# Optimization experiments

Hardware: AMD Instinct MI355X
Metric: run time of the kernel (lower is better)

## Reference

```python
import jax, jax.numpy as jnp
import numpy as np

EPS_NORM = 1e-5
EPS_L2 = 1e-12
SCALE_VALUE = 50.0
FROM_VALUE = 0.4
VALUE_INTERVAL = 0.5


def mvn(x):
    # mean-variance norm per (b, c) over spatial dims; torch .var() is unbiased
    mean = jnp.mean(x, axis=(2, 3), keepdims=True)
    var = jnp.var(x, axis=(2, 3), keepdims=True, ddof=1)
    return (x - mean) / jnp.sqrt(var + EPS_NORM)


def conv1x1(x, W, b):
    # x: [b,c,h,w], W: [out,in], b: [out]
    return jnp.einsum('bchw,oc->bohw', x, W) + b[None, :, None, None]


def setup_inputs() -> dict:
    key = jax.random.key(0)
    ks = jax.random.split(key, 12)
    B, C, Hs, Ws = 4, 512, 64, 64
    HW = Hs * Ws  # 4096 == spatial_dims
    HID = HW // 16
    sc = 1.0 / np.sqrt(C)
    inp = {
        'content': jax.random.normal(ks[0], (B, C, Hs, Ws), jnp.float32),
        'style': jax.random.normal(ks[1], (B, C, Hs, Ws), jnp.float32),
        'Wf': jax.random.normal(ks[2], (C, C), jnp.float32) * sc,
        'bf': jnp.zeros((C,), jnp.float32),
        'Wg': jax.random.normal(ks[3], (C, C), jnp.float32) * sc,
        'bg': jnp.zeros((C,), jnp.float32),
        'Wh': jax.random.normal(ks[4], (C, C), jnp.float32) * sc,
        'bh': jnp.zeros((C,), jnp.float32),
        'Wout': jax.random.normal(ks[5], (C, C), jnp.float32) * sc,
        'bout': jnp.zeros((C,), jnp.float32),
        'W1': jax.random.normal(ks[6], (HID, HW), jnp.float32) * (1.0 / np.sqrt(HW)),
        'b1': jnp.zeros((HID,), jnp.float32),
        'W2': jax.random.normal(ks[7], (1, HID), jnp.float32) * (1.0 / np.sqrt(HID)),
        'b2': jnp.zeros((1,), jnp.float32),
    }
    return inp


def reference(content, style, Wf, bf, Wg, bg, Wh, bh, Wout, bout, W1, b1, W2, b2):
    B, C, H, W = content.shape
    HW = H * W

    Fq = conv1x1(mvn(content), Wf, bf).reshape(B, C, HW)   # query feats
    Gk = conv1x1(mvn(style), Wg, bg).reshape(B, C, HW)      # key feats
    Hv = conv1x1(style, Wh, bh).reshape(B, C, HW)           # value feats

    # affinity matrix: channel-L2-normalized cosine similarity [B, HW_c, HW_s]
    cf = content.reshape(B, C, HW)
    sf = style.reshape(B, C, HW)
    cf = cf / jnp.maximum(jnp.linalg.norm(cf, axis=1, keepdims=True), EPS_L2)
    sf = sf / jnp.maximum(jnp.linalg.norm(sf, axis=1, keepdims=True), EPS_L2)
    A = jnp.einsum('bck,bcl->bkl', cf, sf)

    # attention scores + softmax over style positions
    S = jax.nn.softmax(jnp.einsum('bck,bcl->bkl', Fq, Gk), axis=-1)

    # AEAModule: per-content-pixel adaptive clamp from affinity rows
    hmid = jnp.einsum('bkl,ol->bko', A, W1) + b1            # [B, HW, HID]
    hmid = jax.nn.leaky_relu(hmid, 0.2)
    psi = jax.nn.sigmoid(jnp.einsum('bko,po->bkp', hmid, W2) + b2)  # [B, HW, 1]
    clamp_value = psi * VALUE_INTERVAL + FROM_VALUE
    Sg = jax.nn.sigmoid(SCALE_VALUE * (S - clamp_value))    # gated attention

    # O = H @ Sg^T : [B, C, HW_c]
    O = jnp.einsum('bcl,bkl->bck', Hv, Sg).reshape(B, C, H, W)
    O = conv1x1(O, Wout, bout) + content
    return O
```

## Files before the change

### kernel.cpp

```cpp
#include <hip/hip_runtime.h>

typedef unsigned short u16;
typedef __attribute__((ext_vector_type(8))) short short8;
typedef __attribute__((ext_vector_type(4))) float f32x4;

static constexpr int Bn  = 4;
static constexpr int C   = 512;
static constexpr int HW  = 4096;
static constexpr int HID = 256;

__device__ __forceinline__ float bf2f(u16 u){
  union { unsigned int i; float f; } x; x.i = ((unsigned int)u) << 16; return x.f;
}
__device__ __forceinline__ u16 f2bf(float f){
  union { float f; unsigned int i; } x; x.f = f;
  return (u16)((x.i + 0x7fffu + ((x.i >> 16) & 1u)) >> 16);
}
__device__ __forceinline__ void gld16(const u16* g, u16* l){
  __builtin_amdgcn_global_load_lds((const __attribute__((address_space(1))) void*)g,
                                   (__attribute__((address_space(3))) void*)l, 16, 0, 0);
}

template<bool SPLIT>
__device__ __forceinline__ void mfma_core(const u16* __restrict__ Ah, const u16* __restrict__ Al, int pA,
                                          const u16* __restrict__ Bh, const u16* __restrict__ Bl, int pB,
                                          int K, u16* lds, f32x4 (&acc)[4][4]){
  const int tid  = threadIdx.x;
  const int lane = tid & 63, wave = tid >> 6;
  const int fr = lane & 15, kq = lane >> 4;
  const int kqs = (kq ^ ((fr >> 1) & 3)) * 8;
  const int wm = (wave & 1) * 64, wn = (wave >> 1) * 64;
  constexpr int HB = SPLIT ? 16384 : 8192;
  const int srow = wave*32 + (lane >> 2);
  const int sq   = (((lane & 3) ^ ((lane >> 3) & 3))) * 8;
  const size_t ga = (size_t)srow * pA + sq;
  const size_t gb = (size_t)srow * pB + sq;
  const int ldsc = wave * 1024;

  auto stage = [&](int buf, int k0){
    u16* L = lds + buf*HB;
    #pragma unroll
    for (int i = 0; i < 2; ++i){
      gld16(Ah + ga + (size_t)i*16*pA + k0, L + ldsc + i*512);
      gld16(Bh + gb + (size_t)i*16*pB + k0, L + 4096 + ldsc + i*512);
      if constexpr (SPLIT){
        gld16(Al + ga + (size_t)i*16*pA + k0, L + 8192  + ldsc + i*512);
        gld16(Bl + gb + (size_t)i*16*pB + k0, L + 12288 + ldsc + i*512);
      }
    }
  };
  auto compute = [&](int buf){
    u16* L = lds + buf*HB;
    short8 a[4], b[4];
    #pragma unroll
    for (int i = 0; i < 4; ++i){
      a[i] = *(const short8*)&L[(wm + i*16 + fr)*32 + kqs];
      b[i] = *(const short8*)&L[4096 + (wn + i*16 + fr)*32 + kqs];
    }
    #pragma unroll
    for (int i = 0; i < 4; ++i)
      #pragma unroll
      for (int j = 0; j < 4; ++j)
        acc[i][j] = __builtin_amdgcn_mfma_f32_16x16x32_bf16(a[i], b[j], acc[i][j], 0, 0, 0);
    if constexpr (SPLIT){
      short8 a2[4], b2[4];
      #pragma unroll
      for (int i = 0; i < 4; ++i){
        a2[i] = *(const short8*)&L[8192  + (wm + i*16 + fr)*32 + kqs];
        b2[i] = *(const short8*)&L[12288 + (wn + i*16 + fr)*32 + kqs];
      }
      #pragma unroll
      for (int i = 0; i < 4; ++i)
        #pragma unroll
        for (int j = 0; j < 4; ++j){
          acc[i][j] = __builtin_amdgcn_mfma_f32_16x16x32_bf16(a[i],  b2[j], acc[i][j], 0, 0, 0);
          acc[i][j] = __builtin_amdgcn_mfma_f32_16x16x32_bf16(a2[i], b[j],  acc[i][j], 0, 0, 0);
        }
    }
  };

  stage(0, 0);
  int cur = 0;
  for (int k0 = 32; k0 < K; k0 += 32){
    stage(cur ^ 1, k0);
    if constexpr (SPLIT) asm volatile("s_waitcnt vmcnt(8)" ::: "memory");
    else                 asm volatile("s_waitcnt vmcnt(4)" ::: "memory");
    __builtin_amdgcn_s_barrier();
    compute(cur);
    __builtin_amdgcn_s_barrier();
    cur ^= 1;
  }
  asm volatile("s_waitcnt vmcnt(0)" ::: "memory");
  __builtin_amdgcn_s_barrier();
  compute(cur);
}

struct TileCtx { int wm, wn, cn, rq; };
__device__ __forceinline__ TileCtx tctx(){
  TileCtx t;
  const int wave = threadIdx.x >> 6, lane = threadIdx.x & 63;
  t.wm = blockIdx.y * 128 + (wave & 1) * 64;
  t.wn = blockIdx.x * 128 + (wave >> 1) * 64;
  t.cn = lane & 15; t.rq = (lane >> 4) * 4;
  return t;
}
#define ACC_ZERO(acc) { _Pragma("unroll") for (int i=0;i<4;++i) _Pragma("unroll") for (int j=0;j<4;++j) _Pragma("unroll") for (int r=0;r<4;++r) acc[i][j][r]=0.f; }

__global__ __launch_bounds__(256) void g_conv_split2(const u16* __restrict__ A0h, const u16* __restrict__ A0l,
                                                     const u16* __restrict__ A1h, const u16* __restrict__ A1l,
                                                     const u16* __restrict__ B0h, const u16* __restrict__ B0l,
                                                     const u16* __restrict__ B1h, const u16* __restrict__ B1l,
                                                     const float* __restrict__ bias0, const float* __restrict__ bias1,
                                                     u16* __restrict__ O0h, u16* __restrict__ O0l,
                                                     u16* __restrict__ O1h, u16* __restrict__ O1l,
                                                     size_t bsA, size_t bsO){
  __shared__ u16 lds[32768];
  const int zb = blockIdx.z, b = zb >> 1, z = zb & 1;
  const u16* Ah = (z ? A1h : A0h) + (size_t)b*bsA;  const u16* Al = (z ? A1l : A0l) + (size_t)b*bsA;
  const u16* Bh = z ? B1h : B0h;  const u16* Bl = z ? B1l : B0l;
  const float* bias = z ? bias1 : bias0;
  u16* Ohi = (z ? O1h : O0h) + (size_t)b*bsO;  u16* Olo = (z ? O1l : O0l) + (size_t)b*bsO;
  TileCtx t = tctx();
  f32x4 acc[4][4]; ACC_ZERO(acc);
  mfma_core<true>(Ah + (size_t)blockIdx.y*128*C, Al + (size_t)blockIdx.y*128*C, C,
                  Bh + (size_t)blockIdx.x*128*C, Bl + (size_t)blockIdx.x*128*C, C, C, lds, acc);
  #pragma unroll
  for (int fm = 0; fm < 4; ++fm)
    #pragma unroll
    for (int fn = 0; fn < 4; ++fn)
      #pragma unroll
      for (int r = 0; r < 4; ++r){
        int gm = t.wm + fm*16 + t.rq + r;
        int gn = t.wn + fn*16 + t.cn;
        float v = acc[fm][fn][r] + bias[gn];
        u16 h = f2bf(v);
        Ohi[(size_t)gm*C + gn] = h;
        Olo[(size_t)gm*C + gn] = f2bf(v - bf2f(h));
      }
}

__global__ __launch_bounds__(256) void g_gemm_split_f32(const u16* __restrict__ Ah, const u16* __restrict__ Al, int pA,
                                                        const u16* __restrict__ Bh, const u16* __restrict__ Bl, int pB,
                                                        int K, float* __restrict__ O, int pO,
                                                        size_t bsA, size_t bsB, size_t bsO){
  __shared__ u16 lds[32768];
  const int b = blockIdx.z;
  TileCtx t = tctx();
  f32x4 acc[4][4]; ACC_ZERO(acc);
  mfma_core<true>(Ah + (size_t)b*bsA + (size_t)blockIdx.y*128*pA,
                  Al + (size_t)b*bsA + (size_t)blockIdx.y*128*pA, pA,
                  Bh + (size_t)b*bsB + (size_t)blockIdx.x*128*pB,
                  Bl + (size_t)b*bsB + (size_t)blockIdx.x*128*pB, pB, K, lds, acc);
  float* Ob = O + (size_t)b*bsO;
  #pragma unroll
  for (int fm = 0; fm < 4; ++fm)
    #pragma unroll
    for (int fn = 0; fn < 4; ++fn)
      #pragma unroll
      for (int r = 0; r < 4; ++r)
        Ob[(size_t)(t.wm + fm*16 + t.rq + r)*pO + t.wn + fn*16 + t.cn] = acc[fm][fn][r];
}

__global__ __launch_bounds__(256) void g_gemm_biasm_bf16(const u16* __restrict__ A, int pA,
                                                         const u16* __restrict__ B, int pB,
                                                         int K, const float* __restrict__ bias,
                                                         u16* __restrict__ O, int pO,
                                                         size_t bsB, size_t bsO){
  __shared__ u16 lds[16384];
  const int b = blockIdx.z;
  TileCtx t = tctx();
  f32x4 acc[4][4]; ACC_ZERO(acc);
  mfma_core<false>(A + (size_t)blockIdx.y*128*pA, nullptr, pA,
                   B + (size_t)b*bsB + (size_t)blockIdx.x*128*pB, nullptr, pB, K, lds, acc);
  u16* Ob = O + (size_t)b*bsO;
  #pragma unroll
  for (int fm = 0; fm < 4; ++fm)
    #pragma unroll
    for (int fn = 0; fn < 4; ++fn)
      #pragma unroll
      for (int r = 0; r < 4; ++r){
        int gm = t.wm + fm*16 + t.rq + r;
        Ob[(size_t)gm*pO + t.wn + fn*16 + t.cn] = f2bf(acc[fm][fn][r] + bias[gm]);
      }
}

__global__ __launch_bounds__(256) void g_gemm_plain_bf16(const u16* __restrict__ A, int pA,
                                                         const u16* __restrict__ B, int pB,
                                                         int K, u16* __restrict__ O, int pO,
                                                         size_t bsA, size_t bsB, size_t bsO){
  __shared__ u16 lds[16384];
  const int b = blockIdx.z;
  TileCtx t = tctx();
  f32x4 acc[4][4]; ACC_ZERO(acc);
  mfma_core<false>(A + (size_t)b*bsA + (size_t)blockIdx.y*128*pA, nullptr, pA,
                   B + (size_t)b*bsB + (size_t)blockIdx.x*128*pB, nullptr, pB, K, lds, acc);
  u16* Ob = O + (size_t)b*bsO;
  #pragma unroll
  for (int fm = 0; fm < 4; ++fm)
    #pragma unroll
    for (int fn = 0; fn < 4; ++fn)
      #pragma unroll
      for (int r = 0; r < 4; ++r){
        int gm = t.wm + fm*16 + t.rq + r;
        Ob[(size_t)gm*pO + t.wn + fn*16 + t.cn] = f2bf(acc[fm][fn][r]);
      }
}

__global__ __launch_bounds__(256) void g_gemm_partial(const u16* __restrict__ A, int pA,
                                                      const u16* __restrict__ B, int pB,
                                                      int Kper, float* __restrict__ O, int pO,
                                                      size_t sliceStride, int slices,
                                                      size_t bsB, size_t bsO){
  __shared__ u16 lds[16384];
  const int zz = blockIdx.z;
  const int b = zz / slices, sl = zz - b*slices;
  TileCtx t = tctx();
  const int koff = sl * Kper;
  f32x4 acc[4][4]; ACC_ZERO(acc);
  mfma_core<false>(A + (size_t)blockIdx.y*128*pA + koff, nullptr, pA,
                   B + (size_t)b*bsB + (size_t)blockIdx.x*128*pB + koff, nullptr, pB, Kper, lds, acc);
  float* Oz = O + (size_t)b*bsO + (size_t)sl * sliceStride;
  #pragma unroll
  for (int fm = 0; fm < 4; ++fm)
    #pragma unroll
    for (int fn = 0; fn < 4; ++fn)
      #pragma unroll
      for (int r = 0; r < 4; ++r)
        Oz[(size_t)(t.wm + fm*16 + t.rq + r)*pO + t.wn + fn*16 + t.cn] = acc[fm][fn][r];
}

__global__ __launch_bounds__(256) void k_reduce(const float* __restrict__ in, size_t sliceStride,
                                                int S, u16* __restrict__ out,
                                                size_t bsIn, size_t bsOut){
  const int b = blockIdx.y;
  const float* inb = in + (size_t)b*bsIn;
  u16* outb = out + (size_t)b*bsOut;
  const size_t i4 = ((size_t)blockIdx.x*256 + threadIdx.x) * 4;
  float4 s = *(const float4*)&inb[i4];
  for (int z = 1; z < S; ++z){
    float4 v = *(const float4*)&inb[(size_t)z*sliceStride + i4];
    s.x += v.x; s.y += v.y; s.z += v.z; s.w += v.w;
  }
  u16 r0 = f2bf(s.x), r1 = f2bf(s.y), r2 = f2bf(s.z), r3 = f2bf(s.w);
  uint2 uo; uo.x = (unsigned)r0 | ((unsigned)r1 << 16);
  uo.y = (unsigned)r2 | ((unsigned)r3 << 16);
  *(uint2*)&outb[i4] = uo;
}

__global__ __launch_bounds__(256) void g_gemm_outconv(const u16* __restrict__ A, int pA,
                                                      const u16* __restrict__ B, int pB,
                                                      int K, const float* __restrict__ bias,
                                                      const float* __restrict__ res,
                                                      float* __restrict__ O,
                                                      size_t bsB, size_t bsRes, size_t bsO){
  __shared__ u16 lds[16384];
  const int b = blockIdx.z;
  TileCtx t = tctx();
  f32x4 acc[4][4]; ACC_ZERO(acc);
  mfma_core<false>(A + (size_t)blockIdx.y*128*pA, nullptr, pA,
                   B + (size_t)b*bsB + (size_t)blockIdx.x*128*pB, nullptr, pB, K, lds, acc);
  const float* resb = res + (size_t)b*bsRes;
  float* Ob = O + (size_t)b*bsO;
  #pragma unroll
  for (int fm = 0; fm < 4; ++fm)
    #pragma unroll
    for (int fn = 0; fn < 4; ++fn)
      #pragma unroll
      for (int r = 0; r < 4; ++r){
        int gm = t.wm + fm*16 + t.rq + r;
        int gn = t.wn + fn*16 + t.cn;
        Ob[(size_t)gm*HW + gn] = acc[fm][fn][r] + bias[gm] + resb[(size_t)gm*HW + gn];
      }
}

__global__ __launch_bounds__(256) void g_gemm_hmid(const u16* __restrict__ A, int pA,
                                                   const u16* __restrict__ B, int pB,
                                                   int K, const float* __restrict__ inc,
                                                   const float* __restrict__ b1,
                                                   float* __restrict__ O,
                                                   size_t bsA, size_t bsP, size_t bsInc, size_t bsO){
  __shared__ u16 lds[16384];
  const int b = blockIdx.z;
  TileCtx t = tctx();
  f32x4 acc[4][4]; ACC_ZERO(acc);
  mfma_core<false>(A + (size_t)b*bsA + (size_t)blockIdx.y*128*pA, nullptr, pA,
                   B + (size_t)b*bsP + (size_t)blockIdx.x*128*pB, nullptr, pB, K, lds, acc);
  const float* incb = inc + (size_t)b*bsInc;
  float* Ob = O + (size_t)b*bsO;
  #pragma unroll
  for (int fm = 0; fm < 4; ++fm)
    #pragma unroll
    for (int fn = 0; fn < 4; ++fn)
      #pragma unroll
      for (int r = 0; r < 4; ++r){
        int gm = t.wm + fm*16 + t.rq + r;
        int gn = t.wn + fn*16 + t.cn;
        float h = acc[fm][fn][r] * incb[gm] + b1[gn];
        Ob[(size_t)gm*HID + gn] = (h > 0.f) ? h : 0.2f*h;
      }
}

__global__ __launch_bounds__(256) void k_stats(const float* __restrict__ content,
                                               const float* __restrict__ style,
                                               float2* __restrict__ statsC,
                                               float2* __restrict__ statsS){
  const int bc = blockIdx.x;
  const float* X = (blockIdx.y == 0 ? content : style) + (size_t)bc * HW;
  float s = 0.f, sq = 0.f;
  for (int i = threadIdx.x; i < HW; i += 256){ float v = X[i]; s += v; sq += v*v; }
  __shared__ float rs[256], rq[256];
  rs[threadIdx.x] = s; rq[threadIdx.x] = sq; __syncthreads();
  for (int o = 128; o > 0; o >>= 1){
    if (threadIdx.x < o){ rs[threadIdx.x] += rs[threadIdx.x+o]; rq[threadIdx.x] += rq[threadIdx.x+o]; }
    __syncthreads();
  }
  if (threadIdx.x == 0){
    float mean = rs[0] / (float)HW;
    float var  = (rq[0] - rs[0]*mean) / (float)(HW - 1);
    (blockIdx.y == 0 ? statsC : statsS)[bc] = make_float2(mean, rsqrtf(var + 1e-5f));
  }
}

__global__ __launch_bounds__(256) void k_pixnorm(const float* __restrict__ content,
                                                 const float* __restrict__ style,
                                                 float* __restrict__ inc,
                                                 float* __restrict__ ins){
  const int b = blockIdx.y;
  const int k = blockIdx.x * 256 + threadIdx.x;
  const float* X = (blockIdx.z == 0 ? content : style) + (size_t)b * C * HW + k;
  float acc = 0.f;
  for (int c = 0; c < C; ++c){ float v = X[(size_t)c * HW]; acc += v*v; }
  (blockIdx.z == 0 ? inc : ins)[b*HW + k] = 1.f / fmaxf(sqrtf(acc), 1e-12f);
}

__global__ __launch_bounds__(256) void k_prep2(const float* __restrict__ Xc,
                                               const float* __restrict__ Xs,
                                               const float2* __restrict__ stC,
                                               const float2* __restrict__ stSt,
                                               const float* __restrict__ ins,
                                               u16* __restrict__ ThiC, u16* __restrict__ TloC, u16* __restrict__ TrawC,
                                               u16* __restrict__ ThiS, u16* __restrict__ TloS, u16* __restrict__ TrawS,
                                               u16* __restrict__ stSo,
                                               size_t bsX, size_t bsT, int bsSt, size_t bsIns, size_t bsSo){
  const int zb = blockIdx.z, b = zb >> 1, z = zb & 1;
  const float* X = (z ? Xs : Xc) + (size_t)b*bsX;
  const float2* stats = (z ? stSt : stC) + (size_t)b*bsSt;
  u16* Thi = (z ? ThiS : ThiC) + (size_t)b*bsT;
  u16* Tlo = (z ? TloS : TloC) + (size_t)b*bsT;
  u16* Traw = (z ? TrawS : TrawC) + (size_t)b*bsT;
  u16* sSb = stSo + (size_t)b*bsSo;
  const float* insb = ins + (size_t)b*bsIns;
  __shared__ float tile[64][65];
  __shared__ float2 st[64];
  const int k0 = blockIdx.x*64, c0 = blockIdx.y*64;
  const int t = threadIdx.x;
  if (t < 64) st[t] = stats[c0 + t];
  const int j4 = (t & 15) * 4, i0 = t >> 4;
  float4 sv;
  if (z) sv = *(const float4*)&insb[k0 + j4];
  for (int r = 0; r < 4; ++r){
    int i = i0 + r*16;
    float4 v = *(const float4*)&X[(size_t)(c0+i)*HW + k0 + j4];
    tile[i][j4+0] = v.x; tile[i][j4+1] = v.y; tile[i][j4+2] = v.z; tile[i][j4+3] = v.w;
    if (z){
      u16 q0 = f2bf(v.x*sv.x), q1 = f2bf(v.y*sv.y), q2 = f2bf(v.z*sv.z), q3 = f2bf(v.w*sv.w);
      uint2 uo; uo.x = (unsigned)q0 | ((unsigned)q1 << 16);
      uo.y = (unsigned)q2 | ((unsigned)q3 << 16);
      *(uint2*)&sSb[(size_t)(c0+i)*HW + k0 + j4] = uo;
    }
  }
  __syncthreads();
  const int kk = t >> 2, cc = (t & 3) * 16;
  u16 h[16], l[16], rw[16];
  #pragma unroll
  for (int q = 0; q < 16; ++q){
    float x = tile[cc+q][kk];
    float2 s = st[cc+q];
    rw[q] = f2bf(x);
    float v = (x - s.x) * s.y;
    h[q] = f2bf(v);
    l[q] = f2bf(v - bf2f(h[q]));
  }
  size_t o = (size_t)(k0+kk)*C + c0 + cc;
  #pragma unroll
  for (int q = 0; q < 16; ++q){ Thi[o+q] = h[q]; Tlo[o+q] = l[q]; Traw[o+q] = rw[q]; }
}

__global__ __launch_bounds__(256) void k_wprep(const float* __restrict__ Wf, const float* __restrict__ Wg,
                                               const float* __restrict__ Wh, const float* __restrict__ Wo,
                                               const float* __restrict__ W1,
                                               u16* __restrict__ Wfh, u16* __restrict__ Wfl,
                                               u16* __restrict__ Wgh, u16* __restrict__ Wgl,
                                               u16* __restrict__ Whb, u16* __restrict__ Wob,
                                               u16* __restrict__ W1b){
  const int idx = (blockIdx.x*256 + threadIdx.x) * 4;
  const int mode = blockIdx.y;
  const int nsmall = C*C;
  if (mode == 4){
    float4 v = *(const float4*)&W1[idx];
    W1b[idx+0]=f2bf(v.x); W1b[idx+1]=f2bf(v.y); W1b[idx+2]=f2bf(v.z); W1b[idx+3]=f2bf(v.w);
    return;
  }
  if (idx >= nsmall) return;
  const float* src = (mode==0)?Wf:(mode==1)?Wg:(mode==2)?Wh:Wo;
  float4 v = *(const float4*)&src[idx];
  float vv[4] = {v.x, v.y, v.z, v.w};
  if (mode <= 1){
    u16* oh = (mode==0)?Wfh:Wgh;  u16* ol = (mode==0)?Wfl:Wgl;
    #pragma unroll
    for (int q = 0; q < 4; ++q){
      u16 hh = f2bf(vv[q]);
      oh[idx+q] = hh; ol[idx+q] = f2bf(vv[q] - bf2f(hh));
    }
  } else {
    u16* ob = (mode==2)?Whb:Wob;
    #pragma unroll
    for (int q = 0; q < 4; ++q) ob[idx+q] = f2bf(vv[q]);
  }
}

__global__ __launch_bounds__(256) void k_psi(const float* __restrict__ hmid,
                                             const float* __restrict__ W2,
                                             const float* __restrict__ b2,
                                             float* __restrict__ clampv,
                                             size_t bsH, size_t bsC){
  const int k = blockIdx.x, tid = threadIdx.x, b = blockIdx.y;
  __shared__ float red[256];
  red[tid] = hmid[(size_t)b*bsH + (size_t)k*HID + tid] * W2[tid];
  __syncthreads();
  for (int o = 128; o > 0; o >>= 1){
    if (tid < o) red[tid] += red[tid+o];
    __syncthreads();
  }
  if (tid == 0){
    float psi = 1.f/(1.f + __expf(-(red[0] + b2[0])));
    clampv[(size_t)b*bsC + k] = psi*0.5f + 0.4f;
  }
}

__global__ __launch_bounds__(256) void k_softgate(float* __restrict__ T2,
                                                  const float* __restrict__ clampv,
                                                  size_t bsT, size_t bsC){
  const int k = blockIdx.x, tid = threadIdx.x, b = blockIdx.y;
  float* row = &T2[(size_t)b*bsT + (size_t)k*HW];
  float vals[16];
  float mx = -3.4e38f;
  #pragma unroll
  for (int i = 0; i < 16; ++i){ vals[i] = row[tid + i*256]; mx = fmaxf(mx, vals[i]); }
  __shared__ float red[256];
  red[tid] = mx; __syncthreads();
  for (int o = 128; o > 0; o >>= 1){
    if (tid < o) red[tid] = fmaxf(red[tid], red[tid+o]);
    __syncthreads();
  }
  mx = red[0]; __syncthreads();
  float s = 0.f;
  #pragma unroll
  for (int i = 0; i < 16; ++i){ vals[i] = __expf(vals[i] - mx); s += vals[i]; }
  red[tid] = s; __syncthreads();
  for (int o = 128; o > 0; o >>= 1){
    if (tid < o) red[tid] += red[tid+o];
    __syncthreads();
  }
  const float inv = 1.f / red[0];
  const float cv = clampv[(size_t)b*bsC + k];
  u16* Sg = (u16*)row;
  #pragma unroll
  for (int i = 0; i < 16; ++i){
    float sg = 1.f/(1.f + __expf(-50.f*(vals[i]*inv - cv)));
    Sg[tid + i*256] = f2bf(sg);
  }
}

extern "C" void kernel_launch(void* const* d_in, const int* in_sizes, int n_in,
                              void* d_out, int out_size, void* d_ws, size_t ws_size,
                              hipStream_t stream){
  const float* content = (const float*)d_in[0];
  const float* style   = (const float*)d_in[1];
  const float* Wf   = (const float*)d_in[2];  const float* bfv  = (const float*)d_in[3];
  const float* Wg   = (const float*)d_in[4];  const float* bg   = (const float*)d_in[5];
  const float* Wh   = (const float*)d_in[6];  const float* bh   = (const float*)d_in[7];
  const float* Wo   = (const float*)d_in[8];  const float* bout = (const float*)d_in[9];
  const float* W1   = (const float*)d_in[10]; const float* b1   = (const float*)d_in[11];
  const float* W2   = (const float*)d_in[12]; const float* b2   = (const float*)d_in[13];
  float* out = (float*)d_out;
  (void)in_sizes; (void)n_in; (void)out_size;

  char* ws = (char*)d_ws;
  size_t off = 0;
  auto alloc = [&](size_t bytes)->void*{
    void* p = (void*)(ws + off);
    off += (bytes + 255) & ~(size_t)255;
    return p;
  };
  float2* statsC = (float2*)alloc((size_t)Bn*C*sizeof(float2));
  float2* statsS = (float2*)alloc((size_t)Bn*C*sizeof(float2));
  float*  inc    = (float*) alloc((size_t)Bn*HW*sizeof(float));
  float*  ins    = (float*) alloc((size_t)Bn*HW*sizeof(float));
  float*  clampv = (float*) alloc((size_t)Bn*HW*sizeof(float));
  u16* Wfh = (u16*)alloc((size_t)C*C*2), *Wfl = (u16*)alloc((size_t)C*C*2);
  u16* Wgh = (u16*)alloc((size_t)C*C*2), *Wgl = (u16*)alloc((size_t)C*C*2);
  u16* Whb = (u16*)alloc((size_t)C*C*2), *Wob = (u16*)alloc((size_t)C*C*2);
  u16* W1b = (u16*)alloc((size_t)HID*HW*2);
  const size_t commonEnd = off;

  const size_t TPB = (size_t)HW*C;
  const size_t XB  = (size_t)C*HW;
  const size_t SLB = (size_t)Bn*TPB*2;

  k_stats  <<<dim3(Bn*C, 2),       256, 0, stream>>>(content, style, statsC, statsS);
  k_pixnorm<<<dim3(HW/256, Bn, 2), 256, 0, stream>>>(content, style, inc, ins);
  k_wprep  <<<dim3(HID*HW/1024, 5),256, 0, stream>>>(Wf, Wg, Wh, Wo, W1,
                                                     Wfh, Wfl, Wgh, Wgl, Whb, Wob, W1b);

  auto runPrep = [&](char* R, u16* bFqTh, u16* bFqTl, u16* bGkTh, u16* bGkTl,
                     u16* bHvb, u16* bPT){
    u16* bXcTh = (u16*)(R + 0*SLB);
    u16* bXcTl = (u16*)(R + 1*SLB);
    u16* bXsTh = (u16*)(R + 2*SLB);
    u16* bXsTl = (u16*)(R + 3*SLB);
    u16* bCrT  = (u16*)(R + 4*SLB);
    u16* bSrT  = (u16*)(R + 5*SLB);
    u16* bstS  = (u16*)(R + 6*SLB);
    float* bPpart = (float*)(R + 0*SLB);
    float* bhmid  = (float*)(R + 1*SLB);
    k_prep2 <<<dim3(HW/64, C/64, 2*Bn), 256, 0, stream>>>(content, style, statsC, statsS, ins,
                                                          bXcTh, bXcTl, bCrT, bXsTh, bXsTl, bSrT,
                                                          bstS, XB, TPB, C, HW, TPB);
    g_conv_split2<<<dim3(C/128, HW/128, 2*Bn), 256, 0, stream>>>(
        bXcTh, bXcTl, bXsTh, bXsTl, Wfh, Wfl, Wgh, Wgl, bfv, bg,
        bFqTh, bFqTl, bGkTh, bGkTl, TPB, TPB);
    g_gemm_biasm_bf16<<<dim3(HW/128, C/128, Bn), 256, 0, stream>>>(Whb, C, bSrT, C, C, bh,
                                                                   bHvb, HW, TPB, TPB);
    g_gemm_partial<<<dim3(C/128, HID/128, Bn*8), 256, 0, stream>>>(W1b, HW, bstS, HW, HW/8,
                                                                   bPpart, C, (size_t)HID*C, 8,
                                                                   TPB, (size_t)8*HID*C);
    k_reduce<<<dim3(HID*C/1024, Bn), 256, 0, stream>>>(bPpart, (size_t)HID*C, 8, bPT,
                                                       (size_t)8*HID*C, (size_t)HID*C);
    g_gemm_hmid<<<dim3(HID/128, HW/128, Bn), 256, 0, stream>>>(bCrT, C, bPT, C, C, inc, b1, bhmid,
                                                               TPB, (size_t)HID*C, HW, (size_t)HW*HID);
    k_psi<<<dim3(HW, Bn), 256, 0, stream>>>(bhmid, W2, b2, clampv, (size_t)HW*HID, HW);
  };

  {
    size_t o = commonEnd;
    auto al = [&](size_t bytes)->void*{ void* p = (void*)(ws + o); o += (bytes + 255) & ~(size_t)255; return p; };
    u16* bFqTh = (u16*)al(SLB), *bFqTl = (u16*)al(SLB);
    u16* bGkTh = (u16*)al(SLB), *bGkTl = (u16*)al(SLB);
    u16* bHvb  = (u16*)al(SLB);
    u16* bPT   = (u16*)al((size_t)Bn*HID*C*2);
    u16* bO1T  = (u16*)al(SLB);
    char* R    = (char*)al((size_t)Bn*HW*HW*4);
    if (o <= ws_size){
      runPrep(R, bFqTh, bFqTl, bGkTh, bGkTl, bHvb, bPT);
      float* bT2 = (float*)R;
      g_gemm_split_f32<<<dim3(HW/128, HW/128, Bn), 256, 0, stream>>>(bFqTh, bFqTl, C, bGkTh, bGkTl, C,
                                                                     C, bT2, HW,
                                                                     TPB, TPB, (size_t)HW*HW);
      k_softgate<<<dim3(HW, Bn), 256, 0, stream>>>(bT2, clampv, (size_t)HW*HW, HW);
      g_gemm_plain_bf16<<<dim3(C/128, HW/128, Bn), 256, 0, stream>>>((const u16*)bT2, 2*HW, bHvb, HW,
                                                                     HW, bO1T, C,
                                                                     (size_t)HW*HW*2, TPB, TPB);
      g_gemm_outconv<<<dim3(HW/128, C/128, Bn), 256, 0, stream>>>(Wob, C, bO1T, C, C, bout, content, out,
                                                                  TPB, XB, XB);
      return;
    }
  }

  {
    size_t o = commonEnd;
    auto al = [&](size_t bytes)->void*{ void* p = (void*)(ws + o); o += (bytes + 255) & ~(size_t)255; return p; };
    u16* bFqTh = (u16*)al(SLB), *bFqTl = (u16*)al(SLB);
    u16* bGkTh = (u16*)al(SLB), *bGkTl = (u16*)al(SLB);
    u16* bHvb  = (u16*)al(SLB);
    u16* bPT   = (u16*)al((size_t)Bn*HID*C*2);
    char* R    = (char*)al((size_t)2*HW*HW*4 + (size_t)2*TPB*2 + 256);
    if (o <= ws_size){
      runPrep(R, bFqTh, bFqTl, bGkTh, bGkTl, bHvb, bPT);
      float* T2s  = (float*)R;
      u16*   O1Ts = (u16*)(R + (size_t)2*HW*HW*4);
      for (int cb = 0; cb < Bn; cb += 2){
        g_gemm_split_f32<<<dim3(HW/128, HW/128, 2), 256, 0, stream>>>(
            bFqTh + (size_t)cb*TPB, bFqTl + (size_t)cb*TPB, C,
            bGkTh + (size_t)cb*TPB, bGkTl + (size_t)cb*TPB, C, C, T2s, HW,
            TPB, TPB, (size_t)HW*HW);
        k_softgate<<<dim3(HW, 2), 256, 0, stream>>>(T2s, clampv + (size_t)cb*HW,
                                                    (size_t)HW*HW, HW);
        g_gemm_plain_bf16<<<dim3(C/128, HW/128, 2), 256, 0, stream>>>(
            (const u16*)T2s, 2*HW, bHvb + (size_t)cb*TPB, HW, HW, O1Ts, C,
            (size_t)HW*HW*2, TPB, TPB);
        g_gemm_outconv<<<dim3(HW/128, C/128, 2), 256, 0, stream>>>(
            Wob, C, O1Ts, C, C, bout, content + (size_t)cb*XB, out + (size_t)cb*XB,
            TPB, XB, XB);
      }
      return;
    }
  }

  {
    size_t o = commonEnd;
    auto al = [&](size_t bytes)->void*{ void* p = (void*)(ws + o); o += (bytes + 255) & ~(size_t)255; return p; };
    u16* bFqTh = (u16*)al(SLB), *bFqTl = (u16*)al(SLB);
    u16* bGkTh = (u16*)al(SLB), *bGkTl = (u16*)al(SLB);
    u16* bHvb  = (u16*)al(SLB);
    u16* bPT   = (u16*)al((size_t)Bn*HID*C*2);
    char* R    = (char*)al(7*SLB);
    if (o <= ws_size){
      runPrep(R, bFqTh, bFqTl, bGkTh, bGkTl, bHvb, bPT);
      float* T2s   = (float*)(R + 0*SLB);
      float* Opart = (float*)(R + 4*SLB);
      u16*   O1Ts  = (u16*)  (R + 6*SLB);
      for (int b = 0; b < Bn; ++b){
        g_gemm_split_f32<<<dim3(HW/128, HW/128), 256, 0, stream>>>(
            bFqTh + (size_t)b*TPB, bFqTl + (size_t)b*TPB, C,
            bGkTh + (size_t)b*TPB, bGkTl + (size_t)b*TPB, C, C, T2s, HW, 0, 0, 0);
        k_softgate<<<dim3(HW), 256, 0, stream>>>(T2s, clampv + (size_t)b*HW, 0, 0);
        g_gemm_partial<<<dim3(C/128, HW/128, 4), 256, 0, stream>>>(
            (const u16*)T2s, 2*HW, bHvb + (size_t)b*TPB, HW, 1024,
            Opart, C, (size_t)HW*C, 4, 0, 0);
        k_reduce<<<dim3(HW*C/1024), 256, 0, stream>>>(Opart, (size_t)HW*C, 4, O1Ts, 0, 0);
        g_gemm_outconv<<<dim3(HW/128, C/128), 256, 0, stream>>>(Wob, C, O1Ts, C, C, bout,
            content + (size_t)b*XB, out + (size_t)b*XB, 0, 0, 0);
      }
      return;
    }
  }

  off = commonEnd;
  u16* XcTh = (u16*)alloc((size_t)HW*C*2), *XcTl = (u16*)alloc((size_t)HW*C*2);
  u16* CrT  = (u16*)alloc((size_t)HW*C*2);
  u16* XsTh = (u16*)alloc((size_t)HW*C*2), *XsTl = (u16*)alloc((size_t)HW*C*2);
  u16* SrT  = (u16*)alloc((size_t)HW*C*2);
  u16* stS  = (u16*)alloc((size_t)C*HW*2);
  u16* FqTh = (u16*)alloc((size_t)HW*C*2), *FqTl = (u16*)alloc((size_t)HW*C*2);
  u16* GkTh = (u16*)alloc((size_t)HW*C*2), *GkTl = (u16*)alloc((size_t)HW*C*2);
  u16* Hvb  = (u16*)alloc((size_t)C*HW*2);
  u16* O1T  = (u16*)alloc((size_t)HW*C*2);
  u16* PT   = (u16*)alloc((size_t)HID*C*2);
  float* hmid  = (float*)alloc((size_t)HW*HID*sizeof(float));
  float* Ppart = (float*)alloc((size_t)16*HID*C*sizeof(float));
  float* Opart = (float*)alloc((size_t)4*HW*C*sizeof(float));
  float* T2    = (float*)alloc((size_t)HW*HW*sizeof(float));

  for (int b = 0; b < Bn; ++b){
    const float* cb = content + (size_t)b*C*HW;
    const float* sb = style   + (size_t)b*C*HW;
    const float* incb = inc + (size_t)b*HW;
    const float* insb = ins + (size_t)b*HW;
    float* clb = clampv + (size_t)b*HW;

    k_prep2 <<<dim3(HW/64, C/64, 2), 256, 0, stream>>>(cb, sb, statsC + (size_t)b*C, statsS + (size_t)b*C,
                                                       insb, XcTh, XcTl, CrT, XsTh, XsTl, SrT,
                                                       stS, 0, 0, 0, 0, 0);
    g_conv_split2<<<dim3(C/128, HW/128, 2), 256, 0, stream>>>(
        XcTh, XcTl, XsTh, XsTl, Wfh, Wfl, Wgh, Wgl, bfv, bg,
        FqTh, FqTl, GkTh, GkTl, 0, 0);
    g_gemm_biasm_bf16<<<dim3(HW/128, C/128), 256, 0, stream>>>(Whb, C, SrT, C, C, bh, Hvb, HW, 0, 0);
    g_gemm_partial<<<dim3(C/128, HID/128, 16), 256, 0, stream>>>(W1b, HW, stS, HW, 256,
                                                                 Ppart, C, (size_t)HID*C, 16, 0, 0);
    k_reduce<<<dim3(HID*C/1024), 256, 0, stream>>>(Ppart, (size_t)HID*C, 16, PT, 0, 0);
    g_gemm_hmid<<<dim3(HID/128, HW/128), 256, 0, stream>>>(CrT, C, PT, C, C, incb, b1, hmid, 0, 0, 0, 0);
    k_psi<<<dim3(HW), 256, 0, stream>>>(hmid, W2, b2, clb, 0, 0);
    g_gemm_split_f32<<<dim3(HW/128, HW/128), 256, 0, stream>>>(FqTh, FqTl, C, GkTh, GkTl, C, C, T2, HW, 0, 0, 0);
    k_softgate<<<dim3(HW), 256, 0, stream>>>(T2, clb, 0, 0);
    g_gemm_partial<<<dim3(C/128, HW/128, 4), 256, 0, stream>>>((const u16*)T2, 2*HW, Hvb, HW, 1024,
                                                               Opart, C, (size_t)HW*C, 4, 0, 0);
    k_reduce<<<dim3(HW*C/1024), 256, 0, stream>>>(Opart, (size_t)HW*C, 4, O1T, 0, 0);
    g_gemm_outconv<<<dim3(HW/128, C/128), 256, 0, stream>>>(Wob, C, O1T, C, C, bout, cb,
                                                            out + (size_t)b*C*HW, 0, 0, 0);
  }
}
```

Baseline: 780.5 us.

## Swizzle GEMM tiles, add two-batch attention path, use wave-shuffle reductions

Adds an XCD-aware block swizzle to the split-precision GEMMs. Adds a workspace tier that processes two batches per launch for the attention GEMM, softgate, partial GEMM and reduce. Replaces shared-memory tree reductions in stats, psi and softgate with wave shuffles. Splits the pixel-norm reduction across channel groups and vectorizes the prep stores. The intent is to cut launch count, raise occupancy and improve L2 locality, at the cost of a larger workspace requirement for the new path.

Result: slower. 829.6 us (+6.3%).

```diff
diff --git a/kernel.cpp b/kernel.cpp
--- a/kernel.cpp
+++ b/kernel.cpp
@@ -15,6 +15,25 @@
 __device__ __forceinline__ u16 f2bf(float f){
   union { float f; unsigned int i; } x; x.f = f;
   return (u16)((x.i + 0x7fffu + ((x.i >> 16) & 1u)) >> 16);
+}
+__device__ __forceinline__ float wsum(float v){
+  #pragma unroll
+  for (int o = 32; o > 0; o >>= 1) v += __shfl_xor(v, o, 64);
+  return v;
+}
+__device__ __forceinline__ float wmax(float v){
+  #pragma unroll
+  for (int o = 32; o > 0; o >>= 1) v = fmaxf(v, __shfl_xor(v, o, 64));
+  return v;
+}
+__device__ __forceinline__ uint4 pk8(u16 a,u16 b,u16 c,u16 d,u16 e,u16 f,u16 g,u16 h){
+  uint4 r; r.x=(unsigned)a|((unsigned)b<<16); r.y=(unsigned)c|((unsigned)d<<16);
+  r.z=(unsigned)e|((unsigned)f<<16); r.w=(unsigned)g|((unsigned)h<<16); return r;
+}
+__device__ __forceinline__ int2 xswz(int gx, int gy){
+  int flat = blockIdx.y*gx + blockIdx.x;
+  int w = (flat & 7)*((gx*gy) >> 3) + (flat >> 3);
+  return make_int2(w % gx, w / gx);
 }
 __device__ __forceinline__ void gld16(const u16* g, u16* l){
   __builtin_amdgcn_global_load_lds((const __attribute__((address_space(1))) void*)g,
@@ -96,11 +115,11 @@
 }
 
 struct TileCtx { int wm, wn, cn, rq; };
-__device__ __forceinline__ TileCtx tctx(){
+__device__ __forceinline__ TileCtx tctx(int bx, int by){
   TileCtx t;
   const int wave = threadIdx.x >> 6, lane = threadIdx.x & 63;
-  t.wm = blockIdx.y * 128 + (wave & 1) * 64;
-  t.wn = blockIdx.x * 128 + (wave >> 1) * 64;
+  t.wm = by * 128 + (wave & 1) * 64;
+  t.wn = bx * 128 + (wave >> 1) * 64;
   t.cn = lane & 15; t.rq = (lane >> 4) * 4;
   return t;
 }
@@ -116,14 +135,16 @@
                                                      size_t bsA, size_t bsO){
   __shared__ u16 lds[32768];
   const int zb = blockIdx.z, b = zb >> 1, z = zb & 1;
+  const int2 sw = xswz(gridDim.x, gridDim.y);
+  const int bx = sw.x, by = sw.y;
   const u16* Ah = (z ? A1h : A0h) + (size_t)b*bsA;  const u16* Al = (z ? A1l : A0l) + (size_t)b*bsA;
   const u16* Bh = z ? B1h : B0h;  const u16* Bl = z ? B1l : B0l;
   const float* bias = z ? bias1 : bias0;
   u16* Ohi = (z ? O1h : O0h) + (size_t)b*bsO;  u16* Olo = (z ? O1l : O0l) + (size_t)b*bsO;
-  TileCtx t = tctx();
+  TileCtx t = tctx(bx, by);
   f32x4 acc[4][4]; ACC_ZERO(acc);
-  mfma_core<true>(Ah + (size_t)blockIdx.y*128*C, Al + (size_t)blockIdx.y*128*C, C,
-                  Bh + (size_t)blockIdx.x*128*C, Bl + (size_t)blockIdx.x*128*C, C, C, lds, acc);
+  mfma_core<true>(Ah + (size_t)by*128*C, Al + (size_t)by*128*C, C,
+                  Bh + (size_t)bx*128*C, Bl + (size_t)bx*128*C, C, C, lds, acc);
   #pragma unroll
   for (int fm = 0; fm < 4; ++fm)
     #pragma unroll
@@ -145,12 +166,14 @@
                                                         size_t bsA, size_t bsB, size_t bsO){
   __shared__ u16 lds[32768];
   const int b = blockIdx.z;
-  TileCtx t = tctx();
+  const int2 sw = xswz(gridDim.x, gridDim.y);
+  const int bx = sw.x, by = sw.y;
+  TileCtx t = tctx(bx, by);
   f32x4 acc[4][4]; ACC_ZERO(acc);
-  mfma_core<true>(Ah + (size_t)b*bsA + (size_t)blockIdx.y*128*pA,
-                  Al + (size_t)b*bsA + (size_t)blockIdx.y*128*pA, pA,
-                  Bh + (size_t)b*bsB + (size_t)blockIdx.x*128*pB,
-                  Bl + (size_t)b*bsB + (size_t)blockIdx.x*128*pB, pB, K, lds, acc);
+  mfma_core<true>(Ah + (size_t)b*bsA + (size_t)by*128*pA,
+                  Al + (size_t)b*bsA + (size_t)by*128*pA, pA,
+                  Bh + (size_t)b*bsB + (size_t)bx*128*pB,
+                  Bl + (size_t)b*bsB + (size_t)bx*128*pB, pB, K, lds, acc);
   float* Ob = O + (size_t)b*bsO;
   #pragma unroll
   for (int fm = 0; fm < 4; ++fm)
@@ -168,7 +191,7 @@
                                                          size_t bsB, size_t bsO){
   __shared__ u16 lds[16384];
   const int b = blockIdx.z;
-  TileCtx t = tctx();
+  TileCtx t = tctx(blockIdx.x, blockIdx.y);
   f32x4 acc[4][4]; ACC_ZERO(acc);
   mfma_core<false>(A + (size_t)blockIdx.y*128*pA, nullptr, pA,
                    B + (size_t)b*bsB + (size_t)blockIdx.x*128*pB, nullptr, pB, K, lds, acc);
@@ -190,7 +213,7 @@
                                                          size_t bsA, size_t bsB, size_t bsO){
   __shared__ u16 lds[16384];
   const int b = blockIdx.z;
-  TileCtx t = tctx();
+  TileCtx t = tctx(blockIdx.x, blockIdx.y);
   f32x4 acc[4][4]; ACC_ZERO(acc);
   mfma_core<false>(A + (size_t)b*bsA + (size_t)blockIdx.y*128*pA, nullptr, pA,
                    B + (size_t)b*bsB + (size_t)blockIdx.x*128*pB, nullptr, pB, K, lds, acc);
@@ -210,14 +233,14 @@
                                                       const u16* __restrict__ B, int pB,
                                                       int Kper, float* __restrict__ O, int pO,
                                                       size_t sliceStride, int slices,
-                                                      size_t bsB, size_t bsO){
+                                                      size_t bsA, size_t bsB, size_t bsO){
   __shared__ u16 lds[16384];
   const int zz = blockIdx.z;
   const int b = zz / slices, sl = zz - b*slices;
-  TileCtx t = tctx();
+  TileCtx t = tctx(blockIdx.x, blockIdx.y);
   const int koff = sl * Kper;
   f32x4 acc[4][4]; ACC_ZERO(acc);
-  mfma_core<false>(A + (size_t)blockIdx.y*128*pA + koff, nullptr, pA,
+  mfma_core<false>(A + (size_t)b*bsA + (size_t)blockIdx.y*128*pA + koff, nullptr, pA,
                    B + (size_t)b*bsB + (size_t)blockIdx.x*128*pB + koff, nullptr, pB, Kper, lds, acc);
   float* Oz = O + (size_t)b*bsO + (size_t)sl * sliceStride;
   #pragma unroll
@@ -255,7 +278,7 @@
                                                       size_t bsB, size_t bsRes, size_t bsO){
   __shared__ u16 lds[16384];
   const int b = blockIdx.z;
-  TileCtx t = tctx();
+  TileCtx t = tctx(blockIdx.x, blockIdx.y);
   f32x4 acc[4][4]; ACC_ZERO(acc);
   mfma_core<false>(A + (size_t)blockIdx.y*128*pA, nullptr, pA,
                    B + (size_t)b*bsB + (size_t)blockIdx.x*128*pB, nullptr, pB, K, lds, acc);
@@ -281,7 +304,7 @@
                                                    size_t bsA, size_t bsP, size_t bsInc, size_t bsO){
   __shared__ u16 lds[16384];
   const int b = blockIdx.z;
-  TileCtx t = tctx();
+  TileCtx t = tctx(blockIdx.x, blockIdx.y);
   f32x4 acc[4][4]; ACC_ZERO(acc);
   mfma_core<false>(A + (size_t)b*bsA + (size_t)blockIdx.y*128*pA, nullptr, pA,
                    B + (size_t)b*bsP + (size_t)blockIdx.x*128*pB, nullptr, pB, K, lds, acc);
@@ -308,15 +331,14 @@
   const float* X = (blockIdx.y == 0 ? content : style) + (size_t)bc * HW;
   float s = 0.f, sq = 0.f;
   for (int i = threadIdx.x; i < HW; i += 256){ float v = X[i]; s += v; sq += v*v; }
-  __shared__ float rs[256], rq[256];
-  rs[threadIdx.x] = s; rq[threadIdx.x] = sq; __syncthreads();
-  for (int o = 128; o > 0; o >>= 1){
-    if (threadIdx.x < o){ rs[threadIdx.x] += rs[threadIdx.x+o]; rq[threadIdx.x] += rq[threadIdx.x+o]; }
-    __syncthreads();
-  }
+  s = wsum(s); sq = wsum(sq);
+  __shared__ float as[4], aq[4];
+  if ((threadIdx.x & 63) == 0){ as[threadIdx.x>>6] = s; aq[threadIdx.x>>6] = sq; }
+  __syncthreads();
   if (threadIdx.x == 0){
-    float mean = rs[0] / (float)HW;
-    float var  = (rq[0] - rs[0]*mean) / (float)(HW - 1);
+    float S = as[0]+as[1]+as[2]+as[3], Q = aq[0]+aq[1]+aq[2]+aq[3];
+    float mean = S / (float)HW;
+    float var  = (Q - S*mean) / (float)(HW - 1);
     (blockIdx.y == 0 ? statsC : statsS)[bc] = make_float2(mean, rsqrtf(var + 1e-5f));
   }
 }
@@ -325,12 +347,18 @@
                                                  const float* __restrict__ style,
                                                  float* __restrict__ inc,
                                                  float* __restrict__ ins){
-  const int b = blockIdx.y;
-  const int k = blockIdx.x * 256 + threadIdx.x;
-  const float* X = (blockIdx.z == 0 ? content : style) + (size_t)b * C * HW + k;
+  const int b = blockIdx.y, z = blockIdx.z;
+  const int k0 = blockIdx.x * 64;
+  const int kk = threadIdx.x & 63, cg = threadIdx.x >> 6;
+  const float* X = (z == 0 ? content : style) + (size_t)b * C * HW + k0 + kk;
   float acc = 0.f;
-  for (int c = 0; c < C; ++c){ float v = X[(size_t)c * HW]; acc += v*v; }
-  (blockIdx.z == 0 ? inc : ins)[b*HW + k] = 1.f / fmaxf(sqrtf(acc), 1e-12f);
+  for (int c = cg*128; c < cg*128 + 128; ++c){ float v = X[(size_t)c * HW]; acc += v*v; }
+  __shared__ float part[4][64];
+  part[cg][kk] = acc; __syncthreads();
+  if (threadIdx.x < 64){
+    float t = part[0][kk] + part[1][kk] + part[2][kk] + part[3][kk];
+    (z == 0 ? inc : ins)[b*HW + k0 + kk] = 1.f / fmaxf(sqrtf(t), 1e-12f);
+  }
 }
 
 __global__ __launch_bounds__(256) void k_prep2(const float* __restrict__ Xc,
@@ -382,8 +410,12 @@
     l[q] = f2bf(v - bf2f(h[q]));
   }
   size_t o = (size_t)(k0+kk)*C + c0 + cc;
-  #pragma unroll
-  for (int q = 0; q < 16; ++q){ Thi[o+q] = h[q]; Tlo[o+q] = l[q]; Traw[o+q] = rw[q]; }
+  *(uint4*)&Thi[o]    = pk8(h[0],h[1],h[2],h[3],h[4],h[5],h[6],h[7]);
+  *(uint4*)&Thi[o+8]  = pk8(h[8],h[9],h[10],h[11],h[12],h[13],h[14],h[15]);
+  *(uint4*)&Tlo[o]    = pk8(l[0],l[1],l[2],l[3],l[4],l[5],l[6],l[7]);
+  *(uint4*)&Tlo[o+8]  = pk8(l[8],l[9],l[10],l[11],l[12],l[13],l[14],l[15]);
+  *(uint4*)&Traw[o]   = pk8(rw[0],rw[1],rw[2],rw[3],rw[4],rw[5],rw[6],rw[7]);
+  *(uint4*)&Traw[o+8] = pk8(rw[8],rw[9],rw[10],rw[11],rw[12],rw[13],rw[14],rw[15]);
 }
 
 __global__ __launch_bounds__(256) void k_wprep(const float* __restrict__ Wf, const float* __restrict__ Wg,
@@ -425,15 +457,14 @@
                                              float* __restrict__ clampv,
                                              size_t bsH, size_t bsC){
   const int k = blockIdx.x, tid = threadIdx.x, b = blockIdx.y;
-  __shared__ float red[256];
-  red[tid] = hmid[(size_t)b*bsH + (size_t)k*HID + tid] * W2[tid];
+  float v = hmid[(size_t)b*bsH + (size_t)k*HID + tid] * W2[tid];
+  v = wsum(v);
+  __shared__ float a[4];
+  if ((tid & 63) == 0) a[tid>>6] = v;
   __syncthreads();
-  for (int o = 128; o > 0; o >>= 1){
-    if (tid < o) red[tid] += red[tid+o];
-    __syncthreads();
-  }
   if (tid == 0){
-    float psi = 1.f/(1.f + __expf(-(red[0] + b2[0])));
+    float t = a[0]+a[1]+a[2]+a[3];
+    float psi = 1.f/(1.f + __expf(-(t + b2[0])));
     clampv[(size_t)b*bsC + k] = psi*0.5f + 0.4f;
   }
 }
@@ -447,22 +478,19 @@
   float mx = -3.4e38f;
   #pragma unroll
   for (int i = 0; i < 16; ++i){ vals[i] = row[tid + i*256]; mx = fmaxf(mx, vals[i]); }
-  __shared__ float red[256];
-  red[tid] = mx; __syncthreads();
-  for (int o = 128; o > 0; o >>= 1){
-    if (tid < o) red[tid] = fmaxf(red[tid], red[tid+o]);
-    __syncthreads();
-  }
-  mx = red[0]; __syncthreads();
+  mx = wmax(mx);
+  __shared__ float am[4], asm_[4];
+  if ((tid & 63) == 0) am[tid>>6] = mx;
+  __syncthreads();
+  mx = fmaxf(fmaxf(am[0], am[1]), fmaxf(am[2], am[3]));
   float s = 0.f;
   #pragma unroll
   for (int i = 0; i < 16; ++i){ vals[i] = __expf(vals[i] - mx); s += vals[i]; }
-  red[tid] = s; __syncthreads();
-  for (int o = 128; o > 0; o >>= 1){
-    if (tid < o) red[tid] += red[tid+o];
-    __syncthreads();
-  }
-  const float inv = 1.f / red[0];
+  s = wsum(s);
+  if ((tid & 63) == 0) asm_[tid>>6] = s;
+  __syncthreads();
+  s = asm_[0]+asm_[1]+asm_[2]+asm_[3];
+  const float inv = 1.f / s;
   const float cv = clampv[(size_t)b*bsC + k];
   u16* Sg = (u16*)row;
   #pragma unroll
@@ -509,7 +537,7 @@
   const size_t SLB = (size_t)Bn*TPB*2;
 
   k_stats  <<<dim3(Bn*C, 2),       256, 0, stream>>>(content, style, statsC, statsS);
-  k_pixnorm<<<dim3(HW/256, Bn, 2), 256, 0, stream>>>(content, style, inc, ins);
+  k_pixnorm<<<dim3(HW/64, Bn, 2),  256, 0, stream>>>(content, style, inc, ins);
   k_wprep  <<<dim3(HID*HW/1024, 5),256, 0, stream>>>(Wf, Wg, Wh, Wo, W1,
                                                      Wfh, Wfl, Wgh, Wgl, Whb, Wob, W1b);
 
@@ -532,11 +560,11 @@
         bFqTh, bFqTl, bGkTh, bGkTl, TPB, TPB);
     g_gemm_biasm_bf16<<<dim3(HW/128, C/128, Bn), 256, 0, stream>>>(Whb, C, bSrT, C, C, bh,
                                                                    bHvb, HW, TPB, TPB);
-    g_gemm_partial<<<dim3(C/128, HID/128, Bn*8), 256, 0, stream>>>(W1b, HW, bstS, HW, HW/8,
-                                                                   bPpart, C, (size_t)HID*C, 8,
-                                                                   TPB, (size_t)8*HID*C);
-    k_reduce<<<dim3(HID*C/1024, Bn), 256, 0, stream>>>(bPpart, (size_t)HID*C, 8, bPT,
-                                                       (size_t)8*HID*C, (size_t)HID*C);
+    g_gemm_partial<<<dim3(C/128, HID/128, Bn*16), 256, 0, stream>>>(W1b, HW, bstS, HW, 256,
+                                                                    bPpart, C, (size_t)HID*C, 16,
+                                                                    0, TPB, (size_t)16*HID*C);
+    k_reduce<<<dim3(HID*C/1024, Bn), 256, 0, stream>>>(bPpart, (size_t)HID*C, 16, bPT,
+                                                       (size_t)16*HID*C, (size_t)HID*C);
     g_gemm_hmid<<<dim3(HID/128, HW/128, Bn), 256, 0, stream>>>(bCrT, C, bPT, C, C, inc, b1, bhmid,
                                                                TPB, (size_t)HID*C, HW, (size_t)HW*HID);
     k_psi<<<dim3(HW, Bn), 256, 0, stream>>>(bhmid, W2, b2, clampv, (size_t)HW*HID, HW);
@@ -563,6 +591,40 @@
                                                                      (size_t)HW*HW*2, TPB, TPB);
       g_gemm_outconv<<<dim3(HW/128, C/128, Bn), 256, 0, stream>>>(Wob, C, bO1T, C, C, bout, content, out,
                                                                   TPB, XB, XB);
+      return;
+    }
+  }
+
+  {
+    size_t o = commonEnd;
+    auto al = [&](size_t bytes)->void*{ void* p = (void*)(ws + o); o += (bytes + 255) & ~(size_t)255; return p; };
+    u16* bFqTh = (u16*)al(SLB), *bFqTl = (u16*)al(SLB);
+    u16* bGkTh = (u16*)al(SLB), *bGkTl = (u16*)al(SLB);
+    u16* bHvb  = (u16*)al(SLB);
+    u16* bPT   = (u16*)al((size_t)Bn*HID*C*2);
+    char* R    = (char*)al((size_t)2*HW*HW*4 + (size_t)4*HW*C*4 + (size_t)2*TPB*2);
+    if (o <= ws_size){
+      runPrep(R, bFqTh, bFqTl, bGkTh, bGkTl, bHvb, bPT);
+      float* T2s   = (float*)R;
+      float* Opart = (float*)(R + (size_t)2*HW*HW*4);
+      u16*   O1Ts  = (u16*)(R + (size_t)2*HW*HW*4 + (size_t)4*HW*C*4);
+      for (int cb = 0; cb < Bn; cb += 2){
+        g_gemm_split_f32<<<dim3(HW/128, HW/128, 2), 256, 0, stream>>>(
+            bFqTh + (size_t)cb*TPB, bFqTl + (size_t)cb*TPB, C,
+            bGkTh + (size_t)cb*TPB, bGkTl + (size_t)cb*TPB, C, C, T2s, HW,
+            TPB, TPB, (size_t)HW*HW);
+        k_softgate<<<dim3(HW, 2), 256, 0, stream>>>(T2s, clampv + (size_t)cb*HW,
+                                                    (size_t)HW*HW, HW);
+        g_gemm_partial<<<dim3(C/128, HW/128, 4), 256, 0, stream>>>(
+            (const u16*)T2s, 2*HW, bHvb + (size_t)cb*TPB, HW, 2048,
+            Opart, C, (size_t)HW*C, 2,
+            (size_t)HW*HW*2, TPB, (size_t)2*HW*C);
+        k_reduce<<<dim3(HW*C/1024, 2), 256, 0, stream>>>(Opart, (size_t)HW*C, 2, O1Ts,
+                                                         (size_t)2*HW*C, TPB);
+        g_gemm_outconv<<<dim3(HW/128, C/128, 2), 256, 0, stream>>>(
+            Wob, C, O1Ts, C, C, bout, content + (size_t)cb*XB, out + (size_t)cb*XB,
+            TPB, XB, XB);
+      }
       return;
     }
   }
@@ -617,7 +679,7 @@
         k_softgate<<<dim3(HW), 256, 0, stream>>>(T2s, clampv + (size_t)b*HW, 0, 0);
         g_gemm_partial<<<dim3(C/128, HW/128, 4), 256, 0, stream>>>(
             (const u16*)T2s, 2*HW, bHvb + (size_t)b*TPB, HW, 1024,
-            Opart, C, (size_t)HW*C, 4, 0, 0);
+            Opart, C, (size_t)HW*C, 4, 0, 0, 0);
         k_reduce<<<dim3(HW*C/1024), 256, 0, stream>>>(Opart, (size_t)HW*C, 4, O1Ts, 0, 0);
         g_gemm_outconv<<<dim3(HW/128, C/128), 256, 0, stream>>>(Wob, C, O1Ts, C, C, bout,
             content + (size_t)b*XB, out + (size_t)b*XB, 0, 0, 0);
@@ -657,14 +719,14 @@
         FqTh, FqTl, GkTh, GkTl, 0, 0);
     g_gemm_biasm_bf16<<<dim3(HW/128, C/128), 256, 0, stream>>>(Whb, C, SrT, C, C, bh, Hvb, HW, 0, 0);
     g_gemm_partial<<<dim3(C/128, HID/128, 16), 256, 0, stream>>>(W1b, HW, stS, HW, 256,
-                                                                 Ppart, C, (size_t)HID*C, 16, 0, 0);
+                                                                 Ppart, C, (size_t)HID*C, 16, 0, 0, 0);
     k_reduce<<<dim3(HID*C/1024), 256, 0, stream>>>(Ppart, (size_t)HID*C, 16, PT, 0, 0);
     g_gemm_hmid<<<dim3(HID/128, HW/128), 256, 0, stream>>>(CrT, C, PT, C, C, incb, b1, hmid, 0, 0, 0, 0);
     k_psi<<<dim3(HW), 256, 0, stream>>>(hmid, W2, b2, clb, 0, 0);
     g_gemm_split_f32<<<dim3(HW/128, HW/128), 256, 0, stream>>>(FqTh, FqTl, C, GkTh, GkTl, C, C, T2, HW, 0, 0, 0);
     k_softgate<<<dim3(HW), 256, 0, stream>>>(T2, clb, 0, 0);
     g_gemm_partial<<<dim3(C/128, HW/128, 4), 256, 0, stream>>>((const u16*)T2, 2*HW, Hvb, HW, 1024,
-                                                               Opart, C, (size_t)HW*C, 4, 0, 0);
+                                                               Opart, C, (size_t)HW*C, 4, 0, 0, 0);
     k_reduce<<<dim3(HW*C/1024), 256, 0, stream>>>(Opart, (size_t)HW*C, 4, O1T, 0, 0);
     g_gemm_outconv<<<dim3(HW/128, C/128), 256, 0, stream>>>(Wob, C, O1T, C, C, bout, cb,
                                                             out + (size_t)b*C*HW, 0, 0, 0);
```
